# Kernel tuning notes

Hardware: AMD Instinct MI355X
Metric: run time of the kernel (lower is better)

The kernel has to match this reference:

```python
import jax, jax.numpy as jnp
import numpy as np

LN_EPS = 1e-5   # torch LayerNorm default
NRM_EPS = 1e-8  # normalizer-state epsilon in mLSTMCell


def setup_inputs() -> dict:
    key = jax.random.key(0)
    ks = jax.random.split(key, 3)
    B, T, H, L, O = 32, 256, 1024, 4, 256
    x = jax.random.normal(ks[0], (B, T, H), dtype=jnp.float32)
    # 6 projections per layer in order (q, k, v, i, f, o); Linear stored as [in, out]
    W = jax.random.normal(ks[1], (L, 6, H, H), dtype=jnp.float32) * 0.02
    b = jnp.zeros((L, 6, H), dtype=jnp.float32)
    ln_g = jnp.ones((L, 6, H), dtype=jnp.float32)
    ln_b = jnp.zeros((L, 6, H), dtype=jnp.float32)
    fc_w = jax.random.normal(ks[2], (H, O), dtype=jnp.float32) * 0.02
    fc_b = jnp.zeros((O,), dtype=jnp.float32)
    return {"x": x, "W": W, "b": b, "ln_g": ln_g, "ln_b": ln_b,
            "fc_w": fc_w, "fc_b": fc_b}


def _layer_norm(z, g, beta):
    # z: [6, B, H]; g, beta: [6, H]
    mu = z.mean(-1, keepdims=True)
    var = z.var(-1, keepdims=True)
    return (z - mu) * jax.lax.rsqrt(var + LN_EPS) * g[:, None, :] + beta[:, None, :]


def _cell(x_in, h_prev, c_prev, n_prev, Wl, bl, gl, betal):
    # x_in: [B, H]; states: [B, H]; Wl: [6, H, H]
    z = jnp.einsum('bh,jhd->jbd', x_in, Wl) + bl[:, None, :]
    z = _layer_norm(z, gl, betal)
    q, k, v, zi, zf, zo = z  # q is computed by the original cell but unused
    i = jnp.exp(zi)
    f = jax.nn.sigmoid(zf)
    o = jax.nn.sigmoid(zo)
    # kv_interaction = outer(k, v); sum over dim=1 == sum(k) * v (same math, no [B,H,H])
    kv_sum = k.sum(-1, keepdims=True) * v
    c = f * c_prev + i * kv_sum
    n = f * n_prev + i * k
    n_hat = n / (jnp.linalg.norm(n, axis=-1, keepdims=True) + NRM_EPS)
    h = o * jnp.tanh(c * n_hat)
    return h, c, n


def _mlstm_forward(x, W, b, ln_g, ln_b, fc_w, fc_b):
    B, T, H = x.shape
    L = W.shape[0]
    h0 = jnp.zeros((L, B, H), x.dtype)
    init = (h0, h0, h0)  # (h, c, n)

    def step(carry, x_t):
        h, c, n = carry
        layer_in = x_t
        hs, cs, ns = [], [], []
        for l in range(L):  # small fixed layer count
            h_l, c_l, n_l = _cell(layer_in, h[l], c[l], n[l],
                                  W[l], b[l], ln_g[l], ln_b[l])
            if l > 0:  # residual connection (use_residual=True)
                h_l = h_l + layer_in
            layer_in = h_l
            hs.append(h_l); cs.append(c_l); ns.append(n_l)
        return (jnp.stack(hs), jnp.stack(cs), jnp.stack(ns)), None

    (h, c, n), _ = jax.lax.scan(step, init, jnp.swapaxes(x, 0, 1))
    # output[-1] == top-layer hidden at the final timestep
    out = h[-1] @ fc_w + fc_b  # [B, O]
    return out, (h, c, n)


def reference(x, W, b, ln_g, ln_b, fc_w, fc_b):
    return _mlstm_forward(x, W, b, ln_g, ln_b, fc_w, fc_b)
```

## Files before the change

kernel.cpp:

```cpp
#include <hip/hip_runtime.h>
#include <hip/hip_bf16.h>
#include <math.h>

#define H 1024
#define B 32
#define T 256
#define L 4
#define O 256
#define TCH 128
#define NCHUNK 2
#define SEGLEN 16
#define NSEG (TCH / SEGLEN)

typedef _Float16 half8 __attribute__((ext_vector_type(8)));
typedef _Float16 half4 __attribute__((ext_vector_type(4)));
typedef float f32x4 __attribute__((ext_vector_type(4)));

#define X_PK_OFF   0
#define HB0_OFF    8388608
#define HB1_OFF    16777216
#define WT2_OFF    25165824
#define Z16_OFF    46137344
#define A_OFF      67108864
#define BC_OFF     75497472
#define BN_OFF     83886080
#define STATS_OFF  92274688
#define CARC_OFF   92372992
#define CARN_OFF   92897280
#define STATE_OFF  93421568
#define FCP_OFF    93945856

__global__ __launch_bounds__(256) void pack_w(const float* __restrict__ W,
                                              _Float16* __restrict__ Wt2) {
  int tile = blockIdx.x;
  int m_idx = tile >> 8;
  int kt = (tile >> 4) & 15, ntt = tile & 15;
  int l = m_idx / 5, jj = m_idx % 5;
  const float* Wf = W + ((size_t)(l * 6 + jj + 1) << 20);
  _Float16* out = Wt2 + ((size_t)m_idx << 20);
  __shared__ float ts[64][65];
  int k0 = kt * 64, n0 = ntt * 64;
#pragma unroll
  for (int s = 0; s < 16; ++s) {
    int e = threadIdx.x + s * 256;
    int kk = e >> 6, col = e & 63;
    ts[kk][col] = Wf[(size_t)(k0 + kk) * H + n0 + col];
  }
  __syncthreads();
#pragma unroll
  for (int gi = 0; gi < 2; ++gi) {
    int g = threadIdx.x * 2 + gi;
    int l64 = g & 63, ksl = (g >> 6) & 1, ntl = g >> 7;
    int nn = l64 & 15, kh = l64 >> 4;
    half8 tmp;
#pragma unroll
    for (int e = 0; e < 8; ++e)
      tmp[e] = (_Float16)ts[ksl * 32 + kh * 8 + e][ntl * 16 + nn];
    *(half8*)&out[(size_t)((ntt * 4 + ntl) * 32 + kt * 2 + ksl) * 512 + (size_t)l64 * 8] = tmp;
  }
}

__global__ __launch_bounds__(256) void pack_x(const float* __restrict__ x,
                                              _Float16* __restrict__ x_pk) {
  int t = blockIdx.x;
  __shared__ float ld[32][257];
  for (int c = 0; c < 4; ++c) {
#pragma unroll
    for (int s = 0; s < 32; ++s) {
      int e2 = threadIdx.x + s * 256;
      int b = e2 >> 8, col = e2 & 255;
      ld[b][col] = x[((size_t)b * T + t) * H + c * 256 + col];
    }
    __syncthreads();
#pragma unroll
    for (int s3 = 0; s3 < 4; ++s3) {
      int gg = threadIdx.x * 4 + s3;
      int l64 = gg & 63, ksl = (gg >> 6) & 7, bt = gg >> 9;
      int nn = l64 & 15, kh = l64 >> 4;
      int b = bt * 16 + nn;
      half8 tmp;
#pragma unroll
      for (int e = 0; e < 8; ++e)
        tmp[e] = (_Float16)ld[b][ksl * 32 + kh * 8 + e];
      *(half8*)&x_pk[(size_t)t * 32768 + (size_t)bt * 16384 +
                     (size_t)(c * 8 + ksl) * 512 + (size_t)l64 * 8] = tmp;
    }
    __syncthreads();
  }
}

__global__ __launch_bounds__(512) void gemm_big(
    const _Float16* __restrict__ A_pk, const _Float16* __restrict__ Wl,
    _Float16* __restrict__ z16, int t0) {
  int raw = blockIdx.x;
  int swz = (raw & 7) * 80 + (raw >> 3);
  int bm = swz & 31;
  int bn = swz >> 5;
  int w = threadIdx.x >> 6, lane = threadIdx.x & 63;
  int wm = w >> 2, wn = w & 3;

  __shared__ _Float16 smem[24576];

  int j = bn >> 2;
  const _Float16* gsrc[3];
  int ldst[3];
#pragma unroll
  for (int q = 0; q < 3; ++q) {
    int f = w * 3 + q;
    if (f < 8) {
      gsrc[q] = A_pk + (size_t)(t0 * 2 + bm * 8 + f) * 16384 + lane * 8;
      ldst[q] = f * 512 + lane * 8;
    } else {
      int nf = f - 8;
      gsrc[q] = Wl + ((size_t)j << 20) + (size_t)((bn & 3) * 16 + nf) * 16384 + lane * 8;
      ldst[q] = 4096 + nf * 512 + lane * 8;
    }
  }

  half8 st[3];
#pragma unroll
  for (int q = 0; q < 3; ++q) st[q] = *(const half8*)(gsrc[q]);
#pragma unroll
  for (int q = 0; q < 3; ++q) *(half8*)&smem[ldst[q]] = st[q];
  __syncthreads();

  f32x4 acc[4][4] = {};
  int ardo = wm * 4 * 512 + lane * 8;
  int brdo = 4096 + wn * 4 * 512 + lane * 8;

  for (int ks = 0; ks < 32; ++ks) {
    int cur = (ks & 1) * 12288;
    if (ks + 1 < 32) {
#pragma unroll
      for (int q = 0; q < 3; ++q) st[q] = *(const half8*)(gsrc[q] + (ks + 1) * 512);
    }
    half8 a[4], b[4];
#pragma unroll
    for (int i = 0; i < 4; ++i) a[i] = *(const half8*)&smem[cur + ardo + i * 512];
#pragma unroll
    for (int i = 0; i < 4; ++i) b[i] = *(const half8*)&smem[cur + brdo + i * 512];
#pragma unroll
    for (int i = 0; i < 4; ++i)
#pragma unroll
      for (int jf = 0; jf < 4; ++jf)
        acc[i][jf] = __builtin_amdgcn_mfma_f32_16x16x32_f16(a[i], b[jf], acc[i][jf], 0, 0, 0);
    __syncthreads();
    if (ks + 1 < 32) {
#pragma unroll
      for (int q = 0; q < 3; ++q) *(half8*)&smem[(cur ^ 12288) + ldst[q]] = st[q];
    }
    __syncthreads();
  }

  _Float16 (*cz)[264] = (_Float16(*)[264])smem;
  int hb0 = (bn & 3) * 256;
  for (int p = 0; p < 2; ++p) {
    if (p) __syncthreads();
    if (wm == p) {
#pragma unroll
      for (int i = 0; i < 4; ++i)
#pragma unroll
        for (int jf = 0; jf < 4; ++jf)
#pragma unroll
          for (int r = 0; r < 4; ++r)
            cz[i * 16 + (lane >> 4) * 4 + r][wn * 64 + jf * 16 + (lane & 15)] =
                (_Float16)acc[i][jf][r];
    }
    __syncthreads();
#pragma unroll
    for (int s = 0; s < 4; ++s) {
      int e = threadIdx.x + s * 512;
      int r = e >> 5, h8 = e & 31;
      int m_local = bm * 128 + p * 64 + r;
      half8 vv = *(const half8*)&cz[r][h8 * 8];
      *(half8*)&z16[((size_t)m_local * 5 + j) * 1024 + hb0 + h8 * 8] = vv;
    }
  }
}

__global__ __launch_bounds__(256) void stats_kernel(
    const _Float16* __restrict__ z16, const float* __restrict__ bias,
    const float* __restrict__ ln_g, const float* __restrict__ ln_b,
    float* __restrict__ stats, int l) {
  int row = blockIdx.x, tid = threadIdx.x;
  int h0 = tid * 4;
  float red[13];
#pragma unroll
  for (int jj = 0; jj < 5; ++jj) {
    half4 z4 = *(const half4*)&z16[((size_t)row * 5 + jj) * 1024 + h0];
    float4 bb = *(const float4*)&bias[(size_t)(l * 6 + 1 + jj) * H + h0];
    float vx = (float)z4[0] + bb.x, vy = (float)z4[1] + bb.y,
          vz = (float)z4[2] + bb.z, vw = (float)z4[3] + bb.w;
    red[jj * 2] = vx + vy + vz + vw;
    red[jj * 2 + 1] = vx * vx + vy * vy + vz * vz + vw * vw;
    if (jj == 0) {
      float4 g = *(const float4*)&ln_g[(size_t)(l * 6 + 1) * H + h0];
      float4 be = *(const float4*)&ln_b[(size_t)(l * 6 + 1) * H + h0];
      red[10] = vx * g.x + vy * g.y + vz * g.z + vw * g.w;
      red[11] = g.x + g.y + g.z + g.w;
      red[12] = be.x + be.y + be.z + be.w;
    }
  }
#pragma unroll
  for (int off = 32; off; off >>= 1)
#pragma unroll
    for (int q = 0; q < 13; ++q) red[q] += __shfl_down(red[q], off);
  __shared__ float sb[4][13];
  if ((tid & 63) == 0) {
#pragma unroll
    for (int q = 0; q < 13; ++q) sb[tid >> 6][q] = red[q];
  }
  __syncthreads();
  if (tid == 0) {
    float st[13];
#pragma unroll
    for (int q = 0; q < 13; ++q) st[q] = sb[0][q] + sb[1][q] + sb[2][q] + sb[3][q];
    float* so = stats + (size_t)row * 12;
#pragma unroll
    for (int jj = 0; jj < 5; ++jj) {
      float mu = st[jj * 2] * (1.0f / H);
      float var = st[jj * 2 + 1] * (1.0f / H) - mu * mu;
      so[jj * 2] = mu;
      so[jj * 2 + 1] = rsqrtf(var + 1e-5f);
    }
    float mu0 = st[0] * (1.0f / H);
    float rs0 = rsqrtf(st[1] * (1.0f / H) - mu0 * mu0 + 1e-5f);
    so[10] = rs0 * (st[10] - mu0 * st[11]) + st[12];
    so[11] = 0.f;
  }
}

__global__ __launch_bounds__(256) void scan_p1(
    const _Float16* __restrict__ z16, const float* __restrict__ stats,
    const float* __restrict__ bias, const float* __restrict__ ln_g,
    const float* __restrict__ ln_b, float* __restrict__ Abuf,
    float* __restrict__ Bc, float* __restrict__ Bn, int l) {
  int idx = blockIdx.x * 256 + threadIdx.x;
  int h = idx & 1023;
  int bs = idx >> 10;
  int b = bs & 31, seg = bs >> 5;

  float bz[4], gg[4], bb[4];
#pragma unroll
  for (int jj = 0; jj < 4; ++jj) {
    bz[jj] = bias[(size_t)(l * 6 + 1 + jj) * H + h];
    gg[jj] = ln_g[(size_t)(l * 6 + 1 + jj) * H + h];
    bb[jj] = ln_b[(size_t)(l * 6 + 1 + jj) * H + h];
  }
  float A = 1.f, bc = 0.f, bn = 0.f;
#pragma unroll 2
  for (int u = 0; u < SEGLEN; ++u) {
    int row = (seg * SEGLEN + u) * 32 + b;
    size_t zb = ((size_t)row * 5) * 1024 + h;
    float zk = (float)z16[zb];
    float zv = (float)z16[zb + 1024];
    float zi = (float)z16[zb + 2048];
    float zf = (float)z16[zb + 3072];
    const float* st = stats + (size_t)row * 12;
    float k   = (zk + bz[0] - st[0]) * st[1] * gg[0] + bb[0];
    float v   = (zv + bz[1] - st[2]) * st[3] * gg[1] + bb[1];
    float zi_ = (zi + bz[2] - st[4]) * st[5] * gg[2] + bb[2];
    float zf_ = (zf + bz[3] - st[6]) * st[7] * gg[3] + bb[3];
    float iv = __expf(zi_);
    float fv = 1.f / (1.f + __expf(-zf_));
    A *= fv;
    bn = fv * bn + iv * k;
    bc = fv * bc + iv * (st[10] * v);
    size_t o = (size_t)row * 1024 + h;
    Abuf[o] = A;
    Bn[o] = bn;
    Bc[o] = bc;
  }
}

__global__ __launch_bounds__(256) void scan_p2(
    const float* __restrict__ Abuf, const float* __restrict__ Bc,
    const float* __restrict__ Bn, float* __restrict__ state,
    float* __restrict__ carC, float* __restrict__ carN, int l, int t0) {
  int idx = blockIdx.x * 256 + threadIdx.x;
  int h = idx & 1023, b = idx >> 10;
  size_t sidx = ((size_t)l * B + b) * H + h;
  float cc = 0.f, nn = 0.f;
  if (t0 > 0) {
    cc = state[sidx];
    nn = state[(size_t)L * B * H + sidx];
  }
#pragma unroll
  for (int seg = 0; seg < NSEG; ++seg) {
    size_t coff = (size_t)seg * 32768 + (size_t)b * 1024 + h;
    carC[coff] = cc;
    carN[coff] = nn;
    int rowLast = (seg * SEGLEN + SEGLEN - 1) * 32 + b;
    size_t o = (size_t)rowLast * 1024 + h;
    float a = Abuf[o];
    cc = Bc[o] + a * cc;
    nn = Bn[o] + a * nn;
  }
  state[sidx] = cc;
  state[(size_t)L * B * H + sidx] = nn;
}

__global__ __launch_bounds__(256) void final_kernel(
    const _Float16* __restrict__ z16, const float* __restrict__ stats,
    const float* __restrict__ bias, const float* __restrict__ ln_g,
    const float* __restrict__ ln_b, const float* __restrict__ Abuf,
    const float* __restrict__ Bc, const float* __restrict__ Bn,
    const float* __restrict__ carC, const float* __restrict__ carN,
    const _Float16* __restrict__ hin, _Float16* __restrict__ hout,
    float* __restrict__ out, int l, int t0) {
  int row = blockIdx.x;
  int b = row & 31, tc = row >> 5, t = t0 + tc, seg = tc / SEGLEN;
  int tid = threadIdx.x, h0 = tid * 4;
  size_t o = (size_t)row * 1024 + h0;
  size_t coff = (size_t)seg * 32768 + (size_t)b * 1024 + h0;
  float4 a4 = *(const float4*)&Abuf[o];
  float4 bn4 = *(const float4*)&Bn[o];
  float4 bc4 = *(const float4*)&Bc[o];
  float4 cN = *(const float4*)&carN[coff];
  float4 cC = *(const float4*)&carC[coff];
  float nn[4] = {bn4.x + a4.x * cN.x, bn4.y + a4.y * cN.y,
                 bn4.z + a4.z * cN.z, bn4.w + a4.w * cN.w};
  float cc[4] = {bc4.x + a4.x * cC.x, bc4.y + a4.y * cC.y,
                 bc4.z + a4.z * cC.z, bc4.w + a4.w * cC.w};

  float ss = nn[0] * nn[0] + nn[1] * nn[1] + nn[2] * nn[2] + nn[3] * nn[3];
#pragma unroll
  for (int off = 32; off; off >>= 1) ss += __shfl_down(ss, off);
  __shared__ float sb[4];
  if ((tid & 63) == 0) sb[tid >> 6] = ss;
  __syncthreads();
  float rn = 1.f / (sqrtf(sb[0] + sb[1] + sb[2] + sb[3]) + 1e-8f);

  half4 zo4 = *(const half4*)&z16[((size_t)row * 5 + 4) * 1024 + h0];
  const float* st = stats + (size_t)row * 12;
  float mu = st[8], rs = st[9];
  float4 bz = *(const float4*)&bias[(size_t)(l * 6 + 5) * H + h0];
  float4 g4 = *(const float4*)&ln_g[(size_t)(l * 6 + 5) * H + h0];
  float4 be4 = *(const float4*)&ln_b[(size_t)(l * 6 + 5) * H + h0];
  float gv[4] = {g4.x, g4.y, g4.z, g4.w};
  float bev[4] = {be4.x, be4.y, be4.z, be4.w};
  float zov[4] = {(float)zo4[0] + bz.x, (float)zo4[1] + bz.y,
                  (float)zo4[2] + bz.z, (float)zo4[3] + bz.w};

  size_t hfoff = (size_t)(b >> 4) * 16384 + (size_t)(h0 >> 5) * 512 +
                 (size_t)((((h0 & 31) >> 3) * 16) + (b & 15)) * 8 + (h0 & 7);
  half4 rin;
  if (l > 0) rin = *(const half4*)&hin[(size_t)t * 32768 + hfoff];

  float hh[4];
#pragma unroll
  for (int u = 0; u < 4; ++u) {
    float ov = 1.f / (1.f + __expf(-((zov[u] - mu) * rs * gv[u] + bev[u])));
    float targ = cc[u] * (nn[u] * rn);
    float e2 = __expf(-2.f * fabsf(targ));
    float th = copysignf((1.f - e2) / (1.f + e2), targ);
    hh[u] = ov * th + ((l > 0) ? (float)rin[u] : 0.f);
  }
  half4 hx;
  hx[0] = (_Float16)hh[0]; hx[1] = (_Float16)hh[1];
  hx[2] = (_Float16)hh[2]; hx[3] = (_Float16)hh[3];
  *(half4*)&hout[(size_t)t * 32768 + hfoff] = hx;

  if (t == T - 1) {
    *(float4*)&out[8192 + (size_t)l * 32768 + (size_t)b * 1024 + h0] =
        make_float4(hh[0], hh[1], hh[2], hh[3]);
    *(float4*)&out[8192 + 131072 + ((size_t)(l * B) + b) * 1024 + h0] =
        make_float4(cc[0], cc[1], cc[2], cc[3]);
    *(float4*)&out[8192 + 262144 + ((size_t)(l * B) + b) * 1024 + h0] =
        make_float4(nn[0], nn[1], nn[2], nn[3]);
  }
}

__global__ __launch_bounds__(256) void fc_part(
    const float* __restrict__ out_h, const float* __restrict__ fc_w,
    float* __restrict__ partial) {
  int b = blockIdx.x >> 3, kh = blockIdx.x & 7;
  int o = threadIdx.x;
  const float* hr = out_h + (size_t)b * 1024 + kh * 128;
  const float* wp = fc_w + (size_t)kh * 128 * O + o;
  float acc = 0.f;
#pragma unroll 8
  for (int h = 0; h < 128; ++h)
    acc = fmaf(hr[h], wp[(size_t)h * O], acc);
  partial[((size_t)kh * 32 + b) * O + o] = acc;
}

__global__ __launch_bounds__(256) void fc_reduce(
    const float* __restrict__ partial, const float* __restrict__ fc_b,
    float* __restrict__ out) {
  int b = blockIdx.x, o = threadIdx.x;
  float acc = fc_b[o];
#pragma unroll
  for (int kh = 0; kh < 8; ++kh)
    acc += partial[((size_t)kh * 32 + b) * O + o];
  out[(size_t)b * O + o] = acc;
}

extern "C" void kernel_launch(void* const* d_in, const int* in_sizes, int n_in,
                              void* d_out, int out_size, void* d_ws, size_t ws_size,
                              hipStream_t stream) {
  const float* x    = (const float*)d_in[0];
  const float* W    = (const float*)d_in[1];
  const float* bias = (const float*)d_in[2];
  const float* ln_g = (const float*)d_in[3];
  const float* ln_b = (const float*)d_in[4];
  const float* fc_w = (const float*)d_in[5];
  const float* fc_b = (const float*)d_in[6];
  float* out = (float*)d_out;
  _Float16* wsh = (_Float16*)d_ws;

  _Float16* x_pk = wsh + X_PK_OFF;
  _Float16* hb[2] = {wsh + HB0_OFF, wsh + HB1_OFF};
  _Float16* Wt2  = wsh + WT2_OFF;
  _Float16* z16  = wsh + Z16_OFF;
  float* Abuf  = (float*)(wsh + A_OFF);
  float* Bc    = (float*)(wsh + BC_OFF);
  float* Bn    = (float*)(wsh + BN_OFF);
  float* stats = (float*)(wsh + STATS_OFF);
  float* carC  = (float*)(wsh + CARC_OFF);
  float* carN  = (float*)(wsh + CARN_OFF);
  float* state = (float*)(wsh + STATE_OFF);
  float* fcp   = (float*)(wsh + FCP_OFF);

  pack_w<<<5120, 256, 0, stream>>>(W, Wt2);
  pack_x<<<256, 256, 0, stream>>>(x, x_pk);

  for (int l = 0; l < L; ++l) {
    const _Float16* A_in = (l == 0) ? x_pk : hb[(l - 1) & 1];
    _Float16* h_out = hb[l & 1];
    const _Float16* Wl = Wt2 + ((size_t)(l * 5) << 20);
    for (int c = 0; c < NCHUNK; ++c) {
      int t0 = c * TCH;
      gemm_big<<<640, 512, 0, stream>>>(A_in, Wl, z16, t0);
      stats_kernel<<<4096, 256, 0, stream>>>(z16, bias, ln_g, ln_b, stats, l);
      scan_p1<<<1024, 256, 0, stream>>>(z16, stats, bias, ln_g, ln_b,
                                        Abuf, Bc, Bn, l);
      scan_p2<<<128, 256, 0, stream>>>(Abuf, Bc, Bn, state, carC, carN, l, t0);
      final_kernel<<<4096, 256, 0, stream>>>(z16, stats, bias, ln_g, ln_b,
                                             Abuf, Bc, Bn, carC, carN,
                                             A_in, h_out, out, l, t0);
    }
  }
  fc_part<<<256, 256, 0, stream>>>(out + 8192 + 3 * 32768, fc_w, fcp);
  fc_reduce<<<B, 256, 0, stream>>>(fcp, fc_b, out);
}
```

Measured before the change: 909.6 us.

## Fuse LayerNorm row statistics into GEMM epilogue and use direct global-to-LDS loads

```diff
diff --git a/kernel.cpp b/kernel.cpp
--- a/kernel.cpp
+++ b/kernel.cpp
@@ -29,6 +29,14 @@
 #define CARN_OFF   92897280
 #define STATE_OFF  93421568
 #define FCP_OFF    93945856
+#define PSUM_OFF   94076928
+#define GSUM_OFF   94732288
+
+__device__ __forceinline__ void gll16(const _Float16* g, _Float16* l) {
+  __builtin_amdgcn_global_load_lds(
+      (const __attribute__((address_space(1))) void*)g,
+      (__attribute__((address_space(3))) void*)l, 16, 0, 0);
+}
 
 __global__ __launch_bounds__(256) void pack_w(const float* __restrict__ W,
                                               _Float16* __restrict__ Wt2) {
@@ -89,9 +97,33 @@
   }
 }
 
+__global__ __launch_bounds__(256) void gsum_kernel(
+    const float* __restrict__ ln_g, const float* __restrict__ ln_b,
+    float* __restrict__ gsums) {
+  int l = blockIdx.x;
+  int tid = threadIdx.x;
+  float4 g4 = *(const float4*)&ln_g[(size_t)(l * 6 + 1) * H + tid * 4];
+  float4 b4 = *(const float4*)&ln_b[(size_t)(l * 6 + 1) * H + tid * 4];
+  float sg = g4.x + g4.y + g4.z + g4.w;
+  float sb = b4.x + b4.y + b4.z + b4.w;
+#pragma unroll
+  for (int off = 32; off; off >>= 1) {
+    sg += __shfl_down(sg, off);
+    sb += __shfl_down(sb, off);
+  }
+  __shared__ float sm[8];
+  if ((tid & 63) == 0) { sm[tid >> 6] = sg; sm[(tid >> 6) + 4] = sb; }
+  __syncthreads();
+  if (tid == 0) {
+    gsums[l * 2]     = sm[0] + sm[1] + sm[2] + sm[3];
+    gsums[l * 2 + 1] = sm[4] + sm[5] + sm[6] + sm[7];
+  }
+}
+
 __global__ __launch_bounds__(512) void gemm_big(
     const _Float16* __restrict__ A_pk, const _Float16* __restrict__ Wl,
-    _Float16* __restrict__ z16, int t0) {
+    const float* __restrict__ bias, const float* __restrict__ ln_g,
+    _Float16* __restrict__ z16, float* __restrict__ psum, int l, int t0) {
   int raw = blockIdx.x;
   int swz = (raw & 7) * 80 + (raw >> 3);
   int bm = swz & 31;
@@ -103,36 +135,35 @@
 
   int j = bn >> 2;
   const _Float16* gsrc[3];
-  int ldst[3];
+  int lbase[3];
 #pragma unroll
   for (int q = 0; q < 3; ++q) {
     int f = w * 3 + q;
     if (f < 8) {
       gsrc[q] = A_pk + (size_t)(t0 * 2 + bm * 8 + f) * 16384 + lane * 8;
-      ldst[q] = f * 512 + lane * 8;
+      lbase[q] = f * 512;
     } else {
       int nf = f - 8;
       gsrc[q] = Wl + ((size_t)j << 20) + (size_t)((bn & 3) * 16 + nf) * 16384 + lane * 8;
-      ldst[q] = 4096 + nf * 512 + lane * 8;
-    }
-  }
-
-  half8 st[3];
-#pragma unroll
-  for (int q = 0; q < 3; ++q) st[q] = *(const half8*)(gsrc[q]);
-#pragma unroll
-  for (int q = 0; q < 3; ++q) *(half8*)&smem[ldst[q]] = st[q];
+      lbase[q] = 4096 + nf * 512;
+    }
+  }
+
+#pragma unroll
+  for (int q = 0; q < 3; ++q) gll16(gsrc[q], &smem[lbase[q]]);
   __syncthreads();
 
   f32x4 acc[4][4] = {};
-  int ardo = wm * 4 * 512 + lane * 8;
-  int brdo = 4096 + wn * 4 * 512 + lane * 8;
+  int ardo = wm * 2048 + lane * 8;
+  int brdo = 4096 + wn * 2048 + lane * 8;
 
   for (int ks = 0; ks < 32; ++ks) {
     int cur = (ks & 1) * 12288;
+    int nxt = cur ^ 12288;
     if (ks + 1 < 32) {
 #pragma unroll
-      for (int q = 0; q < 3; ++q) st[q] = *(const half8*)(gsrc[q] + (ks + 1) * 512);
+      for (int q = 0; q < 3; ++q)
+        gll16(gsrc[q] + (ks + 1) * 512, &smem[nxt + lbase[q]]);
     }
     half8 a[4], b[4];
 #pragma unroll
@@ -144,11 +175,6 @@
 #pragma unroll
       for (int jf = 0; jf < 4; ++jf)
         acc[i][jf] = __builtin_amdgcn_mfma_f32_16x16x32_f16(a[i], b[jf], acc[i][jf], 0, 0, 0);
-    __syncthreads();
-    if (ks + 1 < 32) {
-#pragma unroll
-      for (int q = 0; q < 3; ++q) *(half8*)&smem[(cur ^ 12288) + ldst[q]] = st[q];
-    }
     __syncthreads();
   }
 
@@ -175,59 +201,61 @@
       half8 vv = *(const half8*)&cz[r][h8 * 8];
       *(half8*)&z16[((size_t)m_local * 5 + j) * 1024 + hb0 + h8 * 8] = vv;
     }
-  }
-}
-
-__global__ __launch_bounds__(256) void stats_kernel(
-    const _Float16* __restrict__ z16, const float* __restrict__ bias,
-    const float* __restrict__ ln_g, const float* __restrict__ ln_b,
+    {
+      int r = threadIdx.x >> 3;
+      int c0 = (threadIdx.x & 7) * 32;
+      int m_local = bm * 128 + p * 64 + r;
+      const float* bp = bias + (size_t)(l * 6 + 1 + j) * H + hb0 + c0;
+      const float* gp = ln_g + (size_t)(l * 6 + 1) * H + hb0 + c0;
+      float s = 0.f, sq = 0.f, sk = 0.f;
+#pragma unroll 8
+      for (int ci = 0; ci < 32; ++ci) {
+        float val = (float)cz[r][c0 + ci] + bp[ci];
+        s += val;
+        sq += val * val;
+        if (j == 0) sk += val * gp[ci];
+      }
+#pragma unroll
+      for (int off = 4; off; off >>= 1) {
+        s  += __shfl_down(s, off, 8);
+        sq += __shfl_down(sq, off, 8);
+        sk += __shfl_down(sk, off, 8);
+      }
+      if ((threadIdx.x & 7) == 0)
+        *(float4*)&psum[((size_t)bn * 4096 + m_local) * 4] =
+            make_float4(s, sq, sk, 0.f);
+    }
+  }
+}
+
+__global__ __launch_bounds__(256) void stats_finalize(
+    const float* __restrict__ psum, const float* __restrict__ gsums,
     float* __restrict__ stats, int l) {
-  int row = blockIdx.x, tid = threadIdx.x;
-  int h0 = tid * 4;
-  float red[13];
+  int row = blockIdx.x * 256 + threadIdx.x;
+  float* so = stats + (size_t)row * 12;
+  float mu0 = 0.f, rs0 = 0.f;
 #pragma unroll
   for (int jj = 0; jj < 5; ++jj) {
-    half4 z4 = *(const half4*)&z16[((size_t)row * 5 + jj) * 1024 + h0];
-    float4 bb = *(const float4*)&bias[(size_t)(l * 6 + 1 + jj) * H + h0];
-    float vx = (float)z4[0] + bb.x, vy = (float)z4[1] + bb.y,
-          vz = (float)z4[2] + bb.z, vw = (float)z4[3] + bb.w;
-    red[jj * 2] = vx + vy + vz + vw;
-    red[jj * 2 + 1] = vx * vx + vy * vy + vz * vz + vw * vw;
-    if (jj == 0) {
-      float4 g = *(const float4*)&ln_g[(size_t)(l * 6 + 1) * H + h0];
-      float4 be = *(const float4*)&ln_b[(size_t)(l * 6 + 1) * H + h0];
-      red[10] = vx * g.x + vy * g.y + vz * g.z + vw * g.w;
-      red[11] = g.x + g.y + g.z + g.w;
-      red[12] = be.x + be.y + be.z + be.w;
-    }
-  }
-#pragma unroll
-  for (int off = 32; off; off >>= 1)
-#pragma unroll
-    for (int q = 0; q < 13; ++q) red[q] += __shfl_down(red[q], off);
-  __shared__ float sb[4][13];
-  if ((tid & 63) == 0) {
-#pragma unroll
-    for (int q = 0; q < 13; ++q) sb[tid >> 6][q] = red[q];
-  }
-  __syncthreads();
-  if (tid == 0) {
-    float st[13];
-#pragma unroll
-    for (int q = 0; q < 13; ++q) st[q] = sb[0][q] + sb[1][q] + sb[2][q] + sb[3][q];
-    float* so = stats + (size_t)row * 12;
-#pragma unroll
-    for (int jj = 0; jj < 5; ++jj) {
-      float mu = st[jj * 2] * (1.0f / H);
-      float var = st[jj * 2 + 1] * (1.0f / H) - mu * mu;
-      so[jj * 2] = mu;
-      so[jj * 2 + 1] = rsqrtf(var + 1e-5f);
-    }
-    float mu0 = st[0] * (1.0f / H);
-    float rs0 = rsqrtf(st[1] * (1.0f / H) - mu0 * mu0 + 1e-5f);
-    so[10] = rs0 * (st[10] - mu0 * st[11]) + st[12];
-    so[11] = 0.f;
-  }
+    float s = 0.f, sq = 0.f;
+#pragma unroll
+    for (int q = 0; q < 4; ++q) {
+      size_t off = ((size_t)(jj * 4 + q) * 4096 + row) * 4;
+      s += psum[off];
+      sq += psum[off + 1];
+    }
+    float mu = s * (1.0f / H);
+    float var = sq * (1.0f / H) - mu * mu;
+    float rs = rsqrtf(var + 1e-5f);
+    so[jj * 2] = mu;
+    so[jj * 2 + 1] = rs;
+    if (jj == 0) { mu0 = mu; rs0 = rs; }
+  }
+  float sk = 0.f;
+#pragma unroll
+  for (int q = 0; q < 4; ++q)
+    sk += psum[((size_t)q * 4096 + row) * 4 + 2];
+  so[10] = rs0 * (sk - mu0 * gsums[l * 2]) + gsums[l * 2 + 1];
+  so[11] = 0.f;
 }
 
 __global__ __launch_bounds__(256) void scan_p1(
@@ -421,9 +449,12 @@
   float* carN  = (float*)(wsh + CARN_OFF);
   float* state = (float*)(wsh + STATE_OFF);
   float* fcp   = (float*)(wsh + FCP_OFF);
+  float* psum  = (float*)(wsh + PSUM_OFF);
+  float* gsums = (float*)(wsh + GSUM_OFF);
 
   pack_w<<<5120, 256, 0, stream>>>(W, Wt2);
   pack_x<<<256, 256, 0, stream>>>(x, x_pk);
+  gsum_kernel<<<4, 256, 0, stream>>>(ln_g, ln_b, gsums);
 
   for (int l = 0; l < L; ++l) {
     const _Float16* A_in = (l == 0) ? x_pk : hb[(l - 1) & 1];
@@ -431,8 +462,8 @@
     const _Float16* Wl = Wt2 + ((size_t)(l * 5) << 20);
     for (int c = 0; c < NCHUNK; ++c) {
       int t0 = c * TCH;
-      gemm_big<<<640, 512, 0, stream>>>(A_in, Wl, z16, t0);
-      stats_kernel<<<4096, 256, 0, stream>>>(z16, bias, ln_g, ln_b, stats, l);
+      gemm_big<<<640, 512, 0, stream>>>(A_in, Wl, bias, ln_g, z16, psum, l, t0);
+      stats_finalize<<<16, 256, 0, stream>>>(psum, gsums, stats, l);
       scan_p1<<<1024, 256, 0, stream>>>(z16, stats, bias, ln_g, ln_b,
                                         Abuf, Bc, Bn, l);
       scan_p2<<<128, 256, 0, stream>>>(Abuf, Bc, Bn, state, carC, carN, l, t0);
```

After: 1.075 ms. 1.18x slower.

## Deepen GEMM k-loop pipeline with two register stages and one barrier per step

Applied to the files above, without the earlier changes.

```diff
diff --git a/kernel.cpp b/kernel.cpp
--- a/kernel.cpp
+++ b/kernel.cpp
@@ -117,40 +117,68 @@
     }
   }
 
-  half8 st[3];
-#pragma unroll
-  for (int q = 0; q < 3; ++q) st[q] = *(const half8*)(gsrc[q]);
-#pragma unroll
-  for (int q = 0; q < 3; ++q) *(half8*)&smem[ldst[q]] = st[q];
+  half8 stA[3], stB[3];
+#pragma unroll
+  for (int q = 0; q < 3; ++q) stA[q] = *(const half8*)(gsrc[q]);
+#pragma unroll
+  for (int q = 0; q < 3; ++q) *(half8*)&smem[ldst[q]] = stA[q];
+#pragma unroll
+  for (int q = 0; q < 3; ++q) stA[q] = *(const half8*)(gsrc[q] + 512);
   __syncthreads();
 
   f32x4 acc[4][4] = {};
-  int ardo = wm * 4 * 512 + lane * 8;
-  int brdo = 4096 + wn * 4 * 512 + lane * 8;
-
-  for (int ks = 0; ks < 32; ++ks) {
-    int cur = (ks & 1) * 12288;
-    if (ks + 1 < 32) {
-#pragma unroll
-      for (int q = 0; q < 3; ++q) st[q] = *(const half8*)(gsrc[q] + (ks + 1) * 512);
-    }
-    half8 a[4], b[4];
-#pragma unroll
-    for (int i = 0; i < 4; ++i) a[i] = *(const half8*)&smem[cur + ardo + i * 512];
-#pragma unroll
-    for (int i = 0; i < 4; ++i) b[i] = *(const half8*)&smem[cur + brdo + i * 512];
-#pragma unroll
-    for (int i = 0; i < 4; ++i)
-#pragma unroll
-      for (int jf = 0; jf < 4; ++jf)
-        acc[i][jf] = __builtin_amdgcn_mfma_f32_16x16x32_f16(a[i], b[jf], acc[i][jf], 0, 0, 0);
-    __syncthreads();
-    if (ks + 1 < 32) {
-#pragma unroll
-      for (int q = 0; q < 3; ++q) *(half8*)&smem[(cur ^ 12288) + ldst[q]] = st[q];
-    }
-    __syncthreads();
-  }
+  int ardo = wm * 2048 + lane * 8;
+  int brdo = 4096 + wn * 2048 + lane * 8;
+
+  for (int ks = 0; ks < 32; ks += 2) {
+    {
+      if (ks + 2 < 32) {
+#pragma unroll
+        for (int q = 0; q < 3; ++q)
+          stB[q] = *(const half8*)(gsrc[q] + (size_t)(ks + 2) * 512);
+      }
+      half8 a[4], b[4];
+#pragma unroll
+      for (int i = 0; i < 4; ++i) a[i] = *(const half8*)&smem[ardo + i * 512];
+#pragma unroll
+      for (int i = 0; i < 4; ++i) b[i] = *(const half8*)&smem[brdo + i * 512];
+#pragma unroll
+      for (int i = 0; i < 4; ++i)
+#pragma unroll
+        for (int jf = 0; jf < 4; ++jf)
+          acc[i][jf] = __builtin_amdgcn_mfma_f32_16x16x32_f16(a[i], b[jf], acc[i][jf], 0, 0, 0);
+#pragma unroll
+      for (int q = 0; q < 3; ++q) *(half8*)&smem[12288 + ldst[q]] = stA[q];
+      asm volatile("s_waitcnt lgkmcnt(0)" ::: "memory");
+      __builtin_amdgcn_s_barrier();
+      __builtin_amdgcn_sched_barrier(0);
+    }
+    {
+      if (ks + 3 < 32) {
+#pragma unroll
+        for (int q = 0; q < 3; ++q)
+          stA[q] = *(const half8*)(gsrc[q] + (size_t)(ks + 3) * 512);
+      }
+      half8 a[4], b[4];
+#pragma unroll
+      for (int i = 0; i < 4; ++i) a[i] = *(const half8*)&smem[12288 + ardo + i * 512];
+#pragma unroll
+      for (int i = 0; i < 4; ++i) b[i] = *(const half8*)&smem[12288 + brdo + i * 512];
+#pragma unroll
+      for (int i = 0; i < 4; ++i)
+#pragma unroll
+        for (int jf = 0; jf < 4; ++jf)
+          acc[i][jf] = __builtin_amdgcn_mfma_f32_16x16x32_f16(a[i], b[jf], acc[i][jf], 0, 0, 0);
+      if (ks + 2 < 32) {
+#pragma unroll
+        for (int q = 0; q < 3; ++q) *(half8*)&smem[ldst[q]] = stB[q];
+        asm volatile("s_waitcnt lgkmcnt(0)" ::: "memory");
+        __builtin_amdgcn_s_barrier();
+        __builtin_amdgcn_sched_barrier(0);
+      }
+    }
+  }
+  __syncthreads();
 
   _Float16 (*cz)[264] = (_Float16(*)[264])smem;
   int hb0 = (bn & 3) * 256;
```

After: 893.9 us. About the same (-1.7%).
